# Performance work log

Hardware: AMD Instinct MI355X
Metric: run time of the kernel (lower is better)

## Reference

```python
import jax, jax.numpy as jnp
import numpy as np

EMBED_DIM = 1024
HEAD_DIM = 64
B, S = 4, 4096


def setup_inputs() -> dict:
    key = jax.random.key(0)
    ks = jax.random.split(key, 9)
    scale = 1.0 / np.sqrt(EMBED_DIM)
    return {
        "Q": jax.random.normal(ks[0], (B, S, EMBED_DIM), jnp.float32),
        "K": jax.random.normal(ks[1], (B, S, EMBED_DIM), jnp.float32),
        "V": jax.random.normal(ks[2], (B, S, EMBED_DIM), jnp.float32),
        "mask": jnp.ones((1, S, S), jnp.int32),
        "Wq": jax.random.normal(ks[3], (EMBED_DIM, HEAD_DIM), jnp.float32) * scale,
        "bq": jax.random.normal(ks[4], (HEAD_DIM,), jnp.float32) * scale,
        "Wk": jax.random.normal(ks[5], (EMBED_DIM, HEAD_DIM), jnp.float32) * scale,
        "bk": jax.random.normal(ks[6], (HEAD_DIM,), jnp.float32) * scale,
        "Wv": jax.random.normal(ks[7], (EMBED_DIM, HEAD_DIM), jnp.float32) * scale,
        "bv": jax.random.normal(ks[8], (HEAD_DIM,), jnp.float32) * scale,
    }


def reference(Q, K, V, mask, Wq, bq, Wk, bk, Wv, bv):
    # Per-head projections: [B,S,E] @ [E,D] -> [B,S,D]
    q = Q @ Wq + bq
    k = K @ Wk + bk
    v = V @ Wv + bv
    d_k = q.shape[-1]
    # scores: [B,Sq,Sk]
    scores = jnp.einsum("bqd,bkd->bqk", q, k) / jnp.sqrt(jnp.float32(d_k))
    scores = jnp.where(mask == 0, -jnp.inf, scores)
    p_attn = jax.nn.softmax(scores, axis=-1)
    return jnp.einsum("bqk,bkd->bqd", p_attn, v)
```

## Files before the change

### kernel.cpp

```cpp
#include <hip/hip_runtime.h>

#define B_ 4
#define S_ 4096
#define E_ 1024
#define D_ 64

typedef __attribute__((ext_vector_type(8))) short short8;
typedef __attribute__((ext_vector_type(4))) float floatx4;
typedef __attribute__((ext_vector_type(4))) unsigned int uint4v;

__device__ __forceinline__ floatx4 mfma_bf16(short8 a, short8 b, floatx4 c) {
    return __builtin_amdgcn_mfma_f32_16x16x32_bf16(a, b, c, 0, 0, 0);
}

__device__ __forceinline__ short f2bf(float f) {
    unsigned u = __builtin_bit_cast(unsigned, f);
    u = (u + 0x7FFFu + ((u >> 16) & 1u)) >> 16;
    return (short)u;
}

__device__ __forceinline__ unsigned pk2bf(float a, float b) {
    unsigned ua = __builtin_bit_cast(unsigned, a);
    unsigned ub = __builtin_bit_cast(unsigned, b);
    ua = (ua + 0x7FFFu + ((ua >> 16) & 1u)) >> 16;
    ub = (ub + 0x7FFFu + ((ub >> 16) & 1u)) & 0xFFFF0000u;
    return ua | ub;
}

__global__ __launch_bounds__(256) void prep_kernel(
    const float* __restrict__ Wq, const float* __restrict__ Wk, const float* __restrict__ Wv,
    short* __restrict__ WT, int* __restrict__ flag)
{
    int tid = blockIdx.x * 256 + threadIdx.x;
    if (tid == 0) *flag = 0;
    int mat = tid >> 16;
    int rem = tid & 65535;
    const float* W = (mat == 0) ? Wq : ((mat == 1) ? Wk : Wv);
    int n = rem >> 10, k = rem & 1023;
    WT[mat * 65536 + n * E_ + k] = f2bf(W[k * D_ + n]);
}

__global__ __launch_bounds__(256) void maskchk_kernel(
    const int4* __restrict__ mask4, int* __restrict__ flag)
{
    int tid = blockIdx.x * blockDim.x + threadIdx.x;
    int stride = gridDim.x * blockDim.x;
    int found = 0;
    for (int i = tid; i < (S_ * S_ / 4); i += stride) {
        int4 v = mask4[i];
        found |= (v.x == 0) | (v.y == 0) | (v.z == 0) | (v.w == 0);
    }
    if (found) atomicOr(flag, 1);
}

__global__ __launch_bounds__(256, 3) void proj_kernel(
    const float* __restrict__ Qm, const float* __restrict__ Km, const float* __restrict__ Vm,
    const short* __restrict__ WT,
    const float* __restrict__ bq, const float* __restrict__ bk, const float* __restrict__ bv,
    short* __restrict__ qs, short* __restrict__ ks, short* __restrict__ vT)
{
    const int mt = blockIdx.x;
    const int mat = blockIdx.y;
    const int wave = threadIdx.x >> 6;
    const int lane = threadIdx.x & 63;
    const int quad = lane >> 4, c16 = lane & 15;
    const int m0 = mt * 64 + wave * 16;

    const float* X    = (mat == 0) ? Qm : ((mat == 1) ? Km : Vm);
    const float* bias = (mat == 0) ? bq : ((mat == 1) ? bk : bv);
    const short* Wt   = WT + mat * (D_ * E_);

    const float* arow = X + (size_t)(m0 + c16) * E_ + quad * 8;

    floatx4 acc[4];
    #pragma unroll
    for (int f = 0; f < 4; ++f) acc[f] = (floatx4){0.f, 0.f, 0.f, 0.f};

    float4 pa[4], pb[4];
    #pragma unroll
    for (int j = 0; j < 4; ++j) {
        pa[j] = *(const float4*)(arow + j * 32);
        pb[j] = *(const float4*)(arow + j * 32 + 4);
    }

    #pragma unroll 4
    for (int it = 0; it < 32; ++it) {
        float4 ca = pa[it & 3], cb = pb[it & 3];
        if (it < 28) {
            pa[it & 3] = *(const float4*)(arow + (it + 4) * 32);
            pb[it & 3] = *(const float4*)(arow + (it + 4) * 32 + 4);
        }
        uint4v uv;
        uv[0] = pk2bf(ca.x, ca.y); uv[1] = pk2bf(ca.z, ca.w);
        uv[2] = pk2bf(cb.x, cb.y); uv[3] = pk2bf(cb.z, cb.w);
        short8 a = __builtin_bit_cast(short8, uv);
        #pragma unroll
        for (int f = 0; f < 4; ++f) {
            short8 bfr = *(const short8*)(Wt + (size_t)(f * 16 + c16) * E_ + it * 32 + quad * 8);
            acc[f] = mfma_bf16(a, bfr, acc[f]);
        }
    }

    const float scale = (mat == 0) ? (0.125f * 1.4426950408889634f) : 1.0f;
    #pragma unroll
    for (int f = 0; f < 4; ++f) {
        float bb = bias[f * 16 + c16];
        #pragma unroll
        for (int r = 0; r < 4; ++r) {
            int m = m0 + quad * 4 + r;
            float v = (acc[f][r] + bb) * scale;
            short h = f2bf(v);
            if (mat == 0)      qs[(size_t)m * D_ + f * 16 + c16] = h;
            else if (mat == 1) ks[(size_t)m * D_ + f * 16 + c16] = h;
            else vT[((size_t)((m >> 12) * D_ + f * 16 + c16)) * S_ + (m & (S_ - 1))] = h;
        }
    }
}

__global__ __launch_bounds__(512, 2) void flash_kernel(
    const short* __restrict__ qs, const short* __restrict__ ks,
    const short* __restrict__ vT, const int* __restrict__ mask,
    const int* __restrict__ flag, float* __restrict__ out)
{
    __shared__ __align__(16) char smem[35840];
    short* kst = (short*)smem;
    short* pst = kst + 9216;

    const int bid = blockIdx.x;
    const int b  = (bid & 7) >> 1;
    const int qt = ((bid >> 3) << 1) | (bid & 1);
    const int tid = threadIdx.x;
    const int w = tid >> 6;
    const int qw = w & 3, kw = w >> 2;
    const int lane = tid & 63;
    const int quad = lane >> 4, c16 = lane & 15;
    const int m0 = qt * 64 + qw * 16;

    const short* qrow = qs + (size_t)(b * S_ + m0 + c16) * D_ + quad * 8;
    short8 aq0 = *(const short8*)(qrow);
    short8 aq1 = *(const short8*)(qrow + 32);

    const short* kbase = ks + (size_t)b * S_ * D_ + (size_t)kw * 2048 * D_;
    const short* vbase = vT + (size_t)b * D_ * S_ + kw * 2048;

    const int srow = (w & 3) * 8 + (lane >> 3);
    const int schunk = lane & 7;
    const short* gstage = kbase + srow * D_ + schunk * 8;
    short* lstage = kst + kw * 2304 + srow * 72 + schunk * 8;

    floatx4 O[4];
    #pragma unroll
    for (int f = 0; f < 4; ++f) O[f] = (floatx4){0.f, 0.f, 0.f, 0.f};
    float lsum = 0.f;

    const int anyz = *flag;
    short* pw = pst + w * 640;
    short8 g = *(const short8*)(gstage);

    for (int kt = 0; kt < 64; ++kt) {
        const int buf = kt & 1;
        *(short8*)(lstage + buf * 4608) = g;
        short8 gn = g;
        if (kt < 63) gn = *(const short8*)(gstage + (size_t)(kt + 1) * 2048);
        __syncthreads();

        const int key0 = kt * 32;

        short8 vv[4];
        #pragma unroll
        for (int f = 0; f < 4; ++f)
            vv[f] = *(const short8*)(vbase + (size_t)(f * 16 + c16) * S_ + key0 + quad * 8);

        const short* kt_lds = kst + buf * 4608 + kw * 2304;

        floatx4 s[2];
        #pragma unroll
        for (int f = 0; f < 2; ++f) {
            const short* krow = kt_lds + (f * 16 + c16) * 72 + quad * 8;
            short8 ka0 = *(const short8*)(krow);
            short8 ka1 = *(const short8*)(krow + 32);
            floatx4 t = (floatx4){0.f, 0.f, 0.f, 0.f};
            t = mfma_bf16(ka0, aq0, t);
            t = mfma_bf16(ka1, aq1, t);
            s[f] = t;
        }

        if (anyz) {
            #pragma unroll
            for (int f = 0; f < 2; ++f)
                #pragma unroll
                for (int r = 0; r < 4; ++r)
                    if (mask[(size_t)(m0 + c16) * S_ +
                             kw * 2048 + key0 + f * 16 + quad * 4 + r] == 0)
                        s[f][r] = -__builtin_inff();
        }

        #pragma unroll
        for (int f = 0; f < 2; ++f) {
            float p0 = exp2f(s[f][0]), p1 = exp2f(s[f][1]);
            float p2 = exp2f(s[f][2]), p3 = exp2f(s[f][3]);
            lsum += (p0 + p1) + (p2 + p3);
            int2 pk = make_int2((int)pk2bf(p0, p1), (int)pk2bf(p2, p3));
            *(int2*)(pw + c16 * 40 + f * 16 + quad * 4) = pk;
        }

        short8 pa = *(const short8*)(pw + c16 * 40 + quad * 8);

        #pragma unroll
        for (int f = 0; f < 4; ++f) O[f] = mfma_bf16(pa, vv[f], O[f]);
        g = gn;
    }

    lsum += __shfl_xor(lsum, 16);
    lsum += __shfl_xor(lsum, 32);

    __syncthreads();
    float* of = (float*)smem;
    float* lw = (float*)(smem + 34816);
    #pragma unroll
    for (int f = 0; f < 4; ++f)
        #pragma unroll
        for (int r = 0; r < 4; ++r)
            of[(kw * 64 + qw * 16 + quad * 4 + r) * 68 + f * 16 + c16] = O[f][r];
    if (quad == 0) lw[kw * 64 + qw * 16 + c16] = lsum;
    __syncthreads();

    {
        const int q = tid >> 3;
        const int col0 = (tid & 7) * 8;
        const float inv = 1.0f / (lw[q] + lw[64 + q]);
        const float* r0 = &of[q * 68 + col0];
        const float* r1 = &of[(64 + q) * 68 + col0];
        float4 o0, o1;
        o0.x = (r0[0] + r1[0]) * inv; o0.y = (r0[1] + r1[1]) * inv;
        o0.z = (r0[2] + r1[2]) * inv; o0.w = (r0[3] + r1[3]) * inv;
        o1.x = (r0[4] + r1[4]) * inv; o1.y = (r0[5] + r1[5]) * inv;
        o1.z = (r0[6] + r1[6]) * inv; o1.w = (r0[7] + r1[7]) * inv;
        float* op = out + ((size_t)(b * S_ + qt * 64 + q)) * 64 + col0;
        *(float4*)(op) = o0;
        *(float4*)(op + 4) = o1;
    }
}

extern "C" void kernel_launch(void* const* d_in, const int* in_sizes, int n_in,
                              void* d_out, int out_size, void* d_ws, size_t ws_size,
                              hipStream_t stream)
{
    const float* Q   = (const float*)d_in[0];
    const float* K   = (const float*)d_in[1];
    const float* V   = (const float*)d_in[2];
    const int*  mask = (const int*) d_in[3];
    const float* Wq  = (const float*)d_in[4];
    const float* bq  = (const float*)d_in[5];
    const float* Wk  = (const float*)d_in[6];
    const float* bk  = (const float*)d_in[7];
    const float* Wv  = (const float*)d_in[8];
    const float* bv  = (const float*)d_in[9];
    float* out = (float*)d_out;

    short* qs = (short*)d_ws;
    short* ks = qs + (size_t)B_ * S_ * D_;
    short* vT = ks + (size_t)B_ * S_ * D_;
    short* WT = vT + (size_t)B_ * S_ * D_;
    int* flag = (int*)(WT + 3 * D_ * E_);

    prep_kernel<<<768, 256, 0, stream>>>(Wq, Wk, Wv, WT, flag);
    maskchk_kernel<<<2048, 256, 0, stream>>>((const int4*)mask, flag);
    proj_kernel<<<dim3(256, 3), 256, 0, stream>>>(Q, K, V, WT, bq, bk, bv, qs, ks, vT);
    flash_kernel<<<256, 512, 0, stream>>>(qs, ks, vT, mask, flag, out);
}
```

Before: 355.0 us.

## Stage projection tiles via global_load_lds double buffer and fold mask check into proj

Rewrites the projection kernel to stage A (fp32 activations) and W tiles into LDS with direct global-to-LDS loads, using double buffering with XOR-swizzled layouts. Each block now covers 32 rows, and the K dimension is split across wave pairs whose partial sums are reduced through LDS. The separate mask-check kernel is merged in as an extra grid row, which removes one launch and lets the check overlap with projection work. In exchange the kernel now uses more shared memory, needs a barrier every stage and an extra reduction step, and the swizzle indexing is a correctness risk.

```diff
diff --git a/kernel.cpp b/kernel.cpp
--- a/kernel.cpp
+++ b/kernel.cpp
@@ -25,6 +25,12 @@
     ua = (ua + 0x7FFFu + ((ua >> 16) & 1u)) >> 16;
     ub = (ub + 0x7FFFu + ((ub >> 16) & 1u)) & 0xFFFF0000u;
     return ua | ub;
+}
+
+__device__ __forceinline__ void gload_lds16(const void* g, void* l) {
+    __builtin_amdgcn_global_load_lds(
+        (const __attribute__((address_space(1))) void*)g,
+        (__attribute__((address_space(3))) void*)l, 16, 0, 0);
 }
 
 __global__ __launch_bounds__(256) void prep_kernel(
@@ -40,79 +46,116 @@
     WT[mat * 65536 + n * E_ + k] = f2bf(W[k * D_ + n]);
 }
 
-__global__ __launch_bounds__(256) void maskchk_kernel(
-    const int4* __restrict__ mask4, int* __restrict__ flag)
-{
-    int tid = blockIdx.x * blockDim.x + threadIdx.x;
-    int stride = gridDim.x * blockDim.x;
-    int found = 0;
-    for (int i = tid; i < (S_ * S_ / 4); i += stride) {
-        int4 v = mask4[i];
-        found |= (v.x == 0) | (v.y == 0) | (v.z == 0) | (v.w == 0);
-    }
-    if (found) atomicOr(flag, 1);
-}
-
-__global__ __launch_bounds__(256, 3) void proj_kernel(
+__global__ __launch_bounds__(256, 4) void proj_kernel(
     const float* __restrict__ Qm, const float* __restrict__ Km, const float* __restrict__ Vm,
     const short* __restrict__ WT,
     const float* __restrict__ bq, const float* __restrict__ bk, const float* __restrict__ bv,
-    short* __restrict__ qs, short* __restrict__ ks, short* __restrict__ vT)
+    short* __restrict__ qs, short* __restrict__ ks, short* __restrict__ vT,
+    const int4* __restrict__ mask4, int* __restrict__ flag)
 {
-    const int mt = blockIdx.x;
+    if (blockIdx.y == 3) {
+        int tid = blockIdx.x * 256 + threadIdx.x;
+        const int stride = 512 * 256;
+        int found = 0;
+        for (int i = tid; i < (S_ * S_ / 4); i += stride) {
+            int4 v = mask4[i];
+            found |= (v.x == 0) | (v.y == 0) | (v.z == 0) | (v.w == 0);
+        }
+        if (found) atomicOr(flag, 1);
+        return;
+    }
+
+    __shared__ __align__(16) char smem[32768];
+
     const int mat = blockIdx.y;
-    const int wave = threadIdx.x >> 6;
-    const int lane = threadIdx.x & 63;
+    const int bx  = blockIdx.x;
+    const int tid = threadIdx.x;
+    const int w = tid >> 6, lane = tid & 63;
+    const int rt = w & 1, kh = w >> 1;
     const int quad = lane >> 4, c16 = lane & 15;
-    const int m0 = mt * 64 + wave * 16;
+    const int row0 = bx * 32;
 
     const float* X    = (mat == 0) ? Qm : ((mat == 1) ? Km : Vm);
     const float* bias = (mat == 0) ? bq : ((mat == 1) ? bk : bv);
-    const short* Wt   = WT + mat * (D_ * E_);
-
-    const float* arow = X + (size_t)(m0 + c16) * E_ + quad * 8;
+
+    const int slot = w * 64 + lane;
+    const int arow = slot >> 3, ac = slot & 7;
+    const int acs  = ac ^ (arow & 7);
+    const char* gA = (const char*)X + (size_t)(row0 + arow) * 4096 + (size_t)acs * 16;
+    const int wn = slot >> 2, wc = slot & 3;
+    const int wcs = wc ^ ((wn >> 1) & 3);
+    const char* gW = (const char*)(WT + (size_t)mat * 65536) + (size_t)wn * 2048 + (size_t)wcs * 16;
+
+    char* lw = smem + w * 1024;
+
+    #define PSTAGE(buf, s) do {                                   \
+        const char* a0 = gA + (s) * 128;                          \
+        const char* w0 = gW + (s) * 64;                           \
+        char* lb = lw + (buf) * 16384;                            \
+        gload_lds16(a0,        lb);                               \
+        gload_lds16(a0 + 2048, lb + 4096);                        \
+        gload_lds16(w0,        lb + 8192);                        \
+        gload_lds16(w0 + 1024, lb + 12288);                       \
+    } while (0)
 
     floatx4 acc[4];
     #pragma unroll
     for (int f = 0; f < 4; ++f) acc[f] = (floatx4){0.f, 0.f, 0.f, 0.f};
 
-    float4 pa[4], pb[4];
-    #pragma unroll
-    for (int j = 0; j < 4; ++j) {
-        pa[j] = *(const float4*)(arow + j * 32);
-        pb[j] = *(const float4*)(arow + j * 32 + 4);
-    }
-
-    #pragma unroll 4
-    for (int it = 0; it < 32; ++it) {
-        float4 ca = pa[it & 3], cb = pb[it & 3];
-        if (it < 28) {
-            pa[it & 3] = *(const float4*)(arow + (it + 4) * 32);
-            pb[it & 3] = *(const float4*)(arow + (it + 4) * 32 + 4);
-        }
+    const int am = c16 & 7;
+    const int wm = (c16 >> 1) & 3;
+    const char* aAbase = smem + kh * 4096 + (rt * 16 + c16) * 128;
+    const char* aWbase = smem + 8192 + kh * 4096 + c16 * 64 + ((quad ^ wm)) * 16;
+
+    PSTAGE(0, 0);
+    __syncthreads();
+
+    #pragma unroll 2
+    for (int s = 0; s < 16; ++s) {
+        const int buf = s & 1;
+        if (s < 15) PSTAGE(buf ^ 1, s + 1);
+
+        const char* aA = aAbase + buf * 16384;
+        float4 fa = *(const float4*)(aA + (size_t)(((2 * quad)     ^ am) * 16));
+        float4 fb = *(const float4*)(aA + (size_t)(((2 * quad + 1) ^ am) * 16));
         uint4v uv;
-        uv[0] = pk2bf(ca.x, ca.y); uv[1] = pk2bf(ca.z, ca.w);
-        uv[2] = pk2bf(cb.x, cb.y); uv[3] = pk2bf(cb.z, cb.w);
+        uv[0] = pk2bf(fa.x, fa.y); uv[1] = pk2bf(fa.z, fa.w);
+        uv[2] = pk2bf(fb.x, fb.y); uv[3] = pk2bf(fb.z, fb.w);
         short8 a = __builtin_bit_cast(short8, uv);
+
+        const char* aW = aWbase + buf * 16384;
         #pragma unroll
         for (int f = 0; f < 4; ++f) {
-            short8 bfr = *(const short8*)(Wt + (size_t)(f * 16 + c16) * E_ + it * 32 + quad * 8);
-            acc[f] = mfma_bf16(a, bfr, acc[f]);
-        }
-    }
-
-    const float scale = (mat == 0) ? (0.125f * 1.4426950408889634f) : 1.0f;
-    #pragma unroll
-    for (int f = 0; f < 4; ++f) {
-        float bb = bias[f * 16 + c16];
-        #pragma unroll
-        for (int r = 0; r < 4; ++r) {
-            int m = m0 + quad * 4 + r;
-            float v = (acc[f][r] + bb) * scale;
-            short h = f2bf(v);
-            if (mat == 0)      qs[(size_t)m * D_ + f * 16 + c16] = h;
-            else if (mat == 1) ks[(size_t)m * D_ + f * 16 + c16] = h;
-            else vT[((size_t)((m >> 12) * D_ + f * 16 + c16)) * S_ + (m & (S_ - 1))] = h;
+            short8 b = *(const short8*)(aW + (size_t)(f * 16) * 64);
+            acc[f] = mfma_bf16(a, b, acc[f]);
+        }
+        __syncthreads();
+    }
+    #undef PSTAGE
+
+    float* of = (float*)smem;
+    if (kh == 1) {
+        #pragma unroll
+        for (int f = 0; f < 4; ++f)
+            #pragma unroll
+            for (int r = 0; r < 4; ++r)
+                of[(rt * 16 + quad * 4 + r) * 68 + f * 16 + c16] = acc[f][r];
+    }
+    __syncthreads();
+    if (kh == 0) {
+        const float scale = (mat == 0) ? (0.125f * 1.4426950408889634f) : 1.0f;
+        #pragma unroll
+        for (int f = 0; f < 4; ++f) {
+            float bb = bias[f * 16 + c16];
+            #pragma unroll
+            for (int r = 0; r < 4; ++r) {
+                int m = row0 + rt * 16 + quad * 4 + r;
+                float v = (acc[f][r] + of[(rt * 16 + quad * 4 + r) * 68 + f * 16 + c16] + bb) * scale;
+                short h = f2bf(v);
+                if (mat == 0)      qs[(size_t)m * D_ + f * 16 + c16] = h;
+                else if (mat == 1) ks[(size_t)m * D_ + f * 16 + c16] = h;
+                else vT[((size_t)((m >> 12) * D_ + f * 16 + c16)) * S_ + (m & (S_ - 1))] = h;
+            }
         }
     }
 }
@@ -265,7 +308,7 @@
     int* flag = (int*)(WT + 3 * D_ * E_);
 
     prep_kernel<<<768, 256, 0, stream>>>(Wq, Wk, Wv, WT, flag);
-    maskchk_kernel<<<2048, 256, 0, stream>>>((const int4*)mask, flag);
-    proj_kernel<<<dim3(256, 3), 256, 0, stream>>>(Q, K, V, WT, bq, bk, bv, qs, ks, vT);
+    proj_kernel<<<dim3(512, 4), 256, 0, stream>>>(Q, K, V, WT, bq, bk, bv,
+                                                  qs, ks, vT, (const int4*)mask, flag);
     flash_kernel<<<256, 512, 0, stream>>>(qs, ks, vT, mask, flag, out);
 }
```

Measured after the change: 334.5 us. -5.8%, faster.

## Stage projection inputs through LDS with async loads and fuse mask check

Applied to the files above, without the earlier changes.

The projection kernel now streams the fp32 activation rows into a swizzled LDS ring buffer using global_load_lds with a three-stage prefetch and explicit vmcnt waits. Weight fragments are double-buffered in registers. The separate mask-check kernel is folded into the tail of the projection kernel, which removes one launch. Occupancy is raised to 4 blocks per SM. The trade-off is added LDS use and a hand-tuned waitcnt that depends on the exact number of loads in flight.

```diff
diff --git a/kernel.cpp b/kernel.cpp
--- a/kernel.cpp
+++ b/kernel.cpp
@@ -25,6 +25,12 @@
     ua = (ua + 0x7FFFu + ((ua >> 16) & 1u)) >> 16;
     ub = (ub + 0x7FFFu + ((ub >> 16) & 1u)) & 0xFFFF0000u;
     return ua | ub;
+}
+
+__device__ __forceinline__ void gload_lds16(const void* g, void* l) {
+    __builtin_amdgcn_global_load_lds(
+        (const __attribute__((address_space(1))) void*)g,
+        (__attribute__((address_space(3))) void*)l, 16, 0, 0);
 }
 
 __global__ __launch_bounds__(256) void prep_kernel(
@@ -40,66 +46,85 @@
     WT[mat * 65536 + n * E_ + k] = f2bf(W[k * D_ + n]);
 }
 
-__global__ __launch_bounds__(256) void maskchk_kernel(
-    const int4* __restrict__ mask4, int* __restrict__ flag)
-{
-    int tid = blockIdx.x * blockDim.x + threadIdx.x;
-    int stride = gridDim.x * blockDim.x;
-    int found = 0;
-    for (int i = tid; i < (S_ * S_ / 4); i += stride) {
-        int4 v = mask4[i];
-        found |= (v.x == 0) | (v.y == 0) | (v.z == 0) | (v.w == 0);
-    }
-    if (found) atomicOr(flag, 1);
-}
-
-__global__ __launch_bounds__(256, 3) void proj_kernel(
+__global__ __launch_bounds__(256, 4) void proj_kernel(
     const float* __restrict__ Qm, const float* __restrict__ Km, const float* __restrict__ Vm,
     const short* __restrict__ WT,
     const float* __restrict__ bq, const float* __restrict__ bk, const float* __restrict__ bv,
-    short* __restrict__ qs, short* __restrict__ ks, short* __restrict__ vT)
+    short* __restrict__ qs, short* __restrict__ ks, short* __restrict__ vT,
+    const int4* __restrict__ mask4, int* __restrict__ flag)
 {
-    const int mt = blockIdx.x;
+    __shared__ __align__(16) char smem[32768];
+
     const int mat = blockIdx.y;
-    const int wave = threadIdx.x >> 6;
-    const int lane = threadIdx.x & 63;
+    const int bx  = blockIdx.x;
+    const int tid = threadIdx.x;
+    const int wv = tid >> 6, lane = tid & 63;
     const int quad = lane >> 4, c16 = lane & 15;
-    const int m0 = mt * 64 + wave * 16;
+    const int m0 = bx * 64 + wv * 16;
 
     const float* X    = (mat == 0) ? Qm : ((mat == 1) ? Km : Vm);
     const float* bias = (mat == 0) ? bq : ((mat == 1) ? bk : bv);
-    const short* Wt   = WT + mat * (D_ * E_);
-
-    const float* arow = X + (size_t)(m0 + c16) * E_ + quad * 8;
+    const short* Wt   = WT + mat * 65536;
+
+    const int srow = lane >> 3;
+    const int cs   = (lane & 7) ^ srow;
+    const char* gA = (const char*)X + (size_t)(m0 + srow) * 4096 + (size_t)cs * 16;
+    char* lds_w = smem + wv * 8192;
+
+    #define PSTAGE(s) do {                               \
+        const char* a0_ = gA + (size_t)(s) * 128;        \
+        char* lb_ = lds_w + ((s) & 3) * 2048;            \
+        gload_lds16(a0_,         lb_);                   \
+        gload_lds16(a0_ + 32768, lb_ + 1024);            \
+    } while (0)
+
+    const short* wbase = Wt + (size_t)c16 * 1024 + quad * 8;
+    #define WLOAD(s, dst) do {                           \
+        const short* wp_ = wbase + (s) * 32;             \
+        dst[0] = *(const short8*)(wp_);                  \
+        dst[1] = *(const short8*)(wp_ + 16384);          \
+        dst[2] = *(const short8*)(wp_ + 32768);          \
+        dst[3] = *(const short8*)(wp_ + 49152);          \
+    } while (0)
 
     floatx4 acc[4];
     #pragma unroll
     for (int f = 0; f < 4; ++f) acc[f] = (floatx4){0.f, 0.f, 0.f, 0.f};
-
-    float4 pa[4], pb[4];
-    #pragma unroll
-    for (int j = 0; j < 4; ++j) {
-        pa[j] = *(const float4*)(arow + j * 32);
-        pb[j] = *(const float4*)(arow + j * 32 + 4);
-    }
-
-    #pragma unroll 4
-    for (int it = 0; it < 32; ++it) {
-        float4 ca = pa[it & 3], cb = pb[it & 3];
-        if (it < 28) {
-            pa[it & 3] = *(const float4*)(arow + (it + 4) * 32);
-            pb[it & 3] = *(const float4*)(arow + (it + 4) * 32 + 4);
-        }
+    short8 wA[4], wB[4];
+
+    PSTAGE(0); PSTAGE(1); PSTAGE(2);
+    WLOAD(0, wA); WLOAD(1, wB);
+
+    const int am = c16 & 7;
+    const char* ra = smem + wv * 8192 + c16 * 128;
+    const int off0 = ((2 * quad)     ^ am) * 16;
+    const int off1 = ((2 * quad + 1) ^ am) * 16;
+
+    #pragma unroll 2
+    for (int s = 0; s < 32; ++s) {
+        asm volatile("s_waitcnt vmcnt(12)" ::: "memory");
+        if (s + 3 < 32) PSTAGE(s + 3);
+
+        const char* rb = ra + (s & 3) * 2048;
+        float4 fa = *(const float4*)(rb + off0);
+        float4 fb = *(const float4*)(rb + off1);
         uint4v uv;
-        uv[0] = pk2bf(ca.x, ca.y); uv[1] = pk2bf(ca.z, ca.w);
-        uv[2] = pk2bf(cb.x, cb.y); uv[3] = pk2bf(cb.z, cb.w);
+        uv[0] = pk2bf(fa.x, fa.y); uv[1] = pk2bf(fa.z, fa.w);
+        uv[2] = pk2bf(fb.x, fb.y); uv[3] = pk2bf(fb.z, fb.w);
         short8 a = __builtin_bit_cast(short8, uv);
-        #pragma unroll
-        for (int f = 0; f < 4; ++f) {
-            short8 bfr = *(const short8*)(Wt + (size_t)(f * 16 + c16) * E_ + it * 32 + quad * 8);
-            acc[f] = mfma_bf16(a, bfr, acc[f]);
-        }
-    }
+
+        if (s & 1) {
+            #pragma unroll
+            for (int f = 0; f < 4; ++f) acc[f] = mfma_bf16(a, wB[f], acc[f]);
+            if (s + 2 < 32) WLOAD(s + 2, wB);
+        } else {
+            #pragma unroll
+            for (int f = 0; f < 4; ++f) acc[f] = mfma_bf16(a, wA[f], acc[f]);
+            if (s + 2 < 32) WLOAD(s + 2, wA);
+        }
+    }
+    #undef PSTAGE
+    #undef WLOAD
 
     const float scale = (mat == 0) ? (0.125f * 1.4426950408889634f) : 1.0f;
     #pragma unroll
@@ -114,6 +139,17 @@
             else if (mat == 1) ks[(size_t)m * D_ + f * 16 + c16] = h;
             else vT[((size_t)((m >> 12) * D_ + f * 16 + c16)) * S_ + (m & (S_ - 1))] = h;
         }
+    }
+
+    {
+        int btid = (mat * 256 + bx) * 256 + tid;
+        const int stride = 768 * 256;
+        int found = 0;
+        for (int i = btid; i < (S_ * S_ / 4); i += stride) {
+            int4 v = mask4[i];
+            found |= (v.x == 0) | (v.y == 0) | (v.z == 0) | (v.w == 0);
+        }
+        if (found) atomicOr(flag, 1);
     }
 }
 
@@ -265,7 +301,7 @@
     int* flag = (int*)(WT + 3 * D_ * E_);
 
     prep_kernel<<<768, 256, 0, stream>>>(Wq, Wk, Wv, WT, flag);
-    maskchk_kernel<<<2048, 256, 0, stream>>>((const int4*)mask, flag);
-    proj_kernel<<<dim3(256, 3), 256, 0, stream>>>(Q, K, V, WT, bq, bk, bv, qs, ks, vT);
+    proj_kernel<<<dim3(256, 3), 256, 0, stream>>>(Q, K, V, WT, bq, bk, bv,
+                                                  qs, ks, vT, (const int4*)mask, flag);
     flash_kernel<<<256, 512, 0, stream>>>(qs, ks, vT, mask, flag, out);
 }
```

Measured after the change: 348.3 us. Within noise of the previous version (-1.9%).

## Fuse mask check into projection, split-K projection and 4-way key split in flash

Applied to the files above, without the earlier changes.

Removes the separate mask-scan kernel and folds the scan into the tail of the projection kernel. The projection now uses 32-row tiles with a two-way split of the reduction dimension across waves, combined through shared memory, which doubles the block count. The attention kernel now uses 32-query tiles with keys split four ways per block, 512 blocks in total, and a four-way final reduction. The goal is more parallelism and one fewer launch, at the cost of extra LDS traffic and a larger shared-memory footprint.

```diff
diff --git a/kernel.cpp b/kernel.cpp
--- a/kernel.cpp
+++ b/kernel.cpp
@@ -40,80 +40,83 @@
     WT[mat * 65536 + n * E_ + k] = f2bf(W[k * D_ + n]);
 }
 
-__global__ __launch_bounds__(256) void maskchk_kernel(
-    const int4* __restrict__ mask4, int* __restrict__ flag)
-{
-    int tid = blockIdx.x * blockDim.x + threadIdx.x;
-    int stride = gridDim.x * blockDim.x;
-    int found = 0;
-    for (int i = tid; i < (S_ * S_ / 4); i += stride) {
-        int4 v = mask4[i];
-        found |= (v.x == 0) | (v.y == 0) | (v.z == 0) | (v.w == 0);
-    }
-    if (found) atomicOr(flag, 1);
-}
-
-__global__ __launch_bounds__(256, 3) void proj_kernel(
+__global__ __launch_bounds__(256, 4) void proj_kernel(
     const float* __restrict__ Qm, const float* __restrict__ Km, const float* __restrict__ Vm,
     const short* __restrict__ WT,
     const float* __restrict__ bq, const float* __restrict__ bk, const float* __restrict__ bv,
-    short* __restrict__ qs, short* __restrict__ ks, short* __restrict__ vT)
-{
-    const int mt = blockIdx.x;
+    short* __restrict__ qs, short* __restrict__ ks, short* __restrict__ vT,
+    const int4* __restrict__ mask4, int* __restrict__ flag)
+{
+    __shared__ __align__(16) float of[32 * 68];
+
     const int mat = blockIdx.y;
-    const int wave = threadIdx.x >> 6;
-    const int lane = threadIdx.x & 63;
+    const int bx  = blockIdx.x;
+    const int tid = threadIdx.x;
+    const int wv = tid >> 6, lane = tid & 63;
     const int quad = lane >> 4, c16 = lane & 15;
-    const int m0 = mt * 64 + wave * 16;
+    const int rt = wv & 1, kh = wv >> 1;
+    const int m0 = bx * 32 + rt * 16;
 
     const float* X    = (mat == 0) ? Qm : ((mat == 1) ? Km : Vm);
     const float* bias = (mat == 0) ? bq : ((mat == 1) ? bk : bv);
-    const short* Wt   = WT + mat * (D_ * E_);
-
-    const float* arow = X + (size_t)(m0 + c16) * E_ + quad * 8;
+    const short* Wt   = WT + mat * 65536;
+
+    const float* arow = X + (size_t)(m0 + c16) * E_ + kh * 512 + quad * 8;
+    const short* wbase = Wt + (size_t)c16 * E_ + kh * 512 + quad * 8;
 
     floatx4 acc[4];
     #pragma unroll
     for (int f = 0; f < 4; ++f) acc[f] = (floatx4){0.f, 0.f, 0.f, 0.f};
 
-    float4 pa[4], pb[4];
-    #pragma unroll
-    for (int j = 0; j < 4; ++j) {
-        pa[j] = *(const float4*)(arow + j * 32);
-        pb[j] = *(const float4*)(arow + j * 32 + 4);
-    }
-
     #pragma unroll 4
-    for (int it = 0; it < 32; ++it) {
-        float4 ca = pa[it & 3], cb = pb[it & 3];
-        if (it < 28) {
-            pa[it & 3] = *(const float4*)(arow + (it + 4) * 32);
-            pb[it & 3] = *(const float4*)(arow + (it + 4) * 32 + 4);
-        }
+    for (int it = 0; it < 16; ++it) {
+        float4 fa = *(const float4*)(arow + it * 32);
+        float4 fb = *(const float4*)(arow + it * 32 + 4);
         uint4v uv;
-        uv[0] = pk2bf(ca.x, ca.y); uv[1] = pk2bf(ca.z, ca.w);
-        uv[2] = pk2bf(cb.x, cb.y); uv[3] = pk2bf(cb.z, cb.w);
+        uv[0] = pk2bf(fa.x, fa.y); uv[1] = pk2bf(fa.z, fa.w);
+        uv[2] = pk2bf(fb.x, fb.y); uv[3] = pk2bf(fb.z, fb.w);
         short8 a = __builtin_bit_cast(short8, uv);
         #pragma unroll
         for (int f = 0; f < 4; ++f) {
-            short8 bfr = *(const short8*)(Wt + (size_t)(f * 16 + c16) * E_ + it * 32 + quad * 8);
-            acc[f] = mfma_bf16(a, bfr, acc[f]);
-        }
-    }
-
-    const float scale = (mat == 0) ? (0.125f * 1.4426950408889634f) : 1.0f;
-    #pragma unroll
-    for (int f = 0; f < 4; ++f) {
-        float bb = bias[f * 16 + c16];
-        #pragma unroll
-        for (int r = 0; r < 4; ++r) {
-            int m = m0 + quad * 4 + r;
-            float v = (acc[f][r] + bb) * scale;
-            short h = f2bf(v);
-            if (mat == 0)      qs[(size_t)m * D_ + f * 16 + c16] = h;
-            else if (mat == 1) ks[(size_t)m * D_ + f * 16 + c16] = h;
-            else vT[((size_t)((m >> 12) * D_ + f * 16 + c16)) * S_ + (m & (S_ - 1))] = h;
-        }
+            short8 b = *(const short8*)(wbase + (size_t)f * 16384 + it * 32);
+            acc[f] = mfma_bf16(a, b, acc[f]);
+        }
+    }
+
+    if (kh == 1) {
+        #pragma unroll
+        for (int f = 0; f < 4; ++f)
+            #pragma unroll
+            for (int r = 0; r < 4; ++r)
+                of[(rt * 16 + quad * 4 + r) * 68 + f * 16 + c16] = acc[f][r];
+    }
+    __syncthreads();
+    if (kh == 0) {
+        const float scale = (mat == 0) ? (0.125f * 1.4426950408889634f) : 1.0f;
+        #pragma unroll
+        for (int f = 0; f < 4; ++f) {
+            float bb = bias[f * 16 + c16];
+            #pragma unroll
+            for (int r = 0; r < 4; ++r) {
+                int m = m0 + quad * 4 + r;
+                float v = (acc[f][r] + of[(rt * 16 + quad * 4 + r) * 68 + f * 16 + c16] + bb) * scale;
+                short h = f2bf(v);
+                if (mat == 0)      qs[(size_t)m * D_ + f * 16 + c16] = h;
+                else if (mat == 1) ks[(size_t)m * D_ + f * 16 + c16] = h;
+                else vT[((size_t)((m >> 12) * D_ + f * 16 + c16)) * S_ + (m & (S_ - 1))] = h;
+            }
+        }
+    }
+
+    {
+        int btid = (mat * 512 + bx) * 256 + tid;
+        const int stride = 1536 * 256;
+        int found = 0;
+        for (int i = btid; i < (S_ * S_ / 4); i += stride) {
+            int4 v = mask4[i];
+            found |= (v.x == 0) | (v.y == 0) | (v.z == 0) | (v.w == 0);
+        }
+        if (found) atomicOr(flag, 1);
     }
 }
 
@@ -122,31 +125,32 @@
     const short* __restrict__ vT, const int* __restrict__ mask,
     const int* __restrict__ flag, float* __restrict__ out)
 {
-    __shared__ __align__(16) char smem[35840];
+    __shared__ __align__(16) char smem[47104];
     short* kst = (short*)smem;
-    short* pst = kst + 9216;
+    short* pst = kst + 18432;
 
     const int bid = blockIdx.x;
     const int b  = (bid & 7) >> 1;
     const int qt = ((bid >> 3) << 1) | (bid & 1);
     const int tid = threadIdx.x;
     const int w = tid >> 6;
-    const int qw = w & 3, kw = w >> 2;
+    const int qw = w & 1, kwq = w >> 1;
     const int lane = tid & 63;
     const int quad = lane >> 4, c16 = lane & 15;
-    const int m0 = qt * 64 + qw * 16;
+    const int m0 = qt * 32 + qw * 16;
 
     const short* qrow = qs + (size_t)(b * S_ + m0 + c16) * D_ + quad * 8;
     short8 aq0 = *(const short8*)(qrow);
     short8 aq1 = *(const short8*)(qrow + 32);
 
-    const short* kbase = ks + (size_t)b * S_ * D_ + (size_t)kw * 2048 * D_;
-    const short* vbase = vT + (size_t)b * D_ * S_ + kw * 2048;
-
-    const int srow = (w & 3) * 8 + (lane >> 3);
+    const short* kbase = ks + (size_t)b * S_ * D_;
+    const short* vbase = vT + (size_t)b * D_ * S_ + kwq * 1024;
+
+    const int sq   = w >> 1;
+    const int srow = (w & 1) * 16 + (lane >> 3);
     const int schunk = lane & 7;
-    const short* gstage = kbase + srow * D_ + schunk * 8;
-    short* lstage = kst + kw * 2304 + srow * 72 + schunk * 8;
+    const short* gstage = kbase + ((size_t)sq * 1024 + srow) * D_ + schunk * 8;
+    short* lstage = kst + sq * 2304 + srow * 72 + schunk * 8;
 
     floatx4 O[4];
     #pragma unroll
@@ -155,13 +159,18 @@
 
     const int anyz = *flag;
     short* pw = pst + w * 640;
-    short8 g = *(const short8*)(gstage);
-
-    for (int kt = 0; kt < 64; ++kt) {
+    short8 g0 = *(const short8*)(gstage);
+    short8 g1 = *(const short8*)(gstage + 8 * D_);
+
+    for (int kt = 0; kt < 32; ++kt) {
         const int buf = kt & 1;
-        *(short8*)(lstage + buf * 4608) = g;
-        short8 gn = g;
-        if (kt < 63) gn = *(const short8*)(gstage + (size_t)(kt + 1) * 2048);
+        *(short8*)(lstage + buf * 9216)           = g0;
+        *(short8*)(lstage + buf * 9216 + 8 * 72)  = g1;
+        short8 gn0 = g0, gn1 = g1;
+        if (kt < 31) {
+            gn0 = *(const short8*)(gstage + (size_t)(kt + 1) * 2048);
+            gn1 = *(const short8*)(gstage + (size_t)(kt + 1) * 2048 + 8 * D_);
+        }
         __syncthreads();
 
         const int key0 = kt * 32;
@@ -171,7 +180,7 @@
         for (int f = 0; f < 4; ++f)
             vv[f] = *(const short8*)(vbase + (size_t)(f * 16 + c16) * S_ + key0 + quad * 8);
 
-        const short* kt_lds = kst + buf * 4608 + kw * 2304;
+        const short* kt_lds = kst + buf * 9216 + kwq * 2304;
 
         floatx4 s[2];
         #pragma unroll
@@ -191,7 +200,7 @@
                 #pragma unroll
                 for (int r = 0; r < 4; ++r)
                     if (mask[(size_t)(m0 + c16) * S_ +
-                             kw * 2048 + key0 + f * 16 + quad * 4 + r] == 0)
+                             kwq * 1024 + key0 + f * 16 + quad * 4 + r] == 0)
                         s[f][r] = -__builtin_inff();
         }
 
@@ -208,7 +217,7 @@
 
         #pragma unroll
         for (int f = 0; f < 4; ++f) O[f] = mfma_bf16(pa, vv[f], O[f]);
-        g = gn;
+        g0 = gn0; g1 = gn1;
     }
 
     lsum += __shfl_xor(lsum, 16);
@@ -221,24 +230,22 @@
     for (int f = 0; f < 4; ++f)
         #pragma unroll
         for (int r = 0; r < 4; ++r)
-            of[(kw * 64 + qw * 16 + quad * 4 + r) * 68 + f * 16 + c16] = O[f][r];
-    if (quad == 0) lw[kw * 64 + qw * 16 + c16] = lsum;
+            of[(kwq * 32 + qw * 16 + quad * 4 + r) * 68 + f * 16 + c16] = O[f][r];
+    if (quad == 0) lw[kwq * 32 + qw * 16 + c16] = lsum;
     __syncthreads();
 
     {
-        const int q = tid >> 3;
-        const int col0 = (tid & 7) * 8;
-        const float inv = 1.0f / (lw[q] + lw[64 + q]);
-        const float* r0 = &of[q * 68 + col0];
-        const float* r1 = &of[(64 + q) * 68 + col0];
-        float4 o0, o1;
-        o0.x = (r0[0] + r1[0]) * inv; o0.y = (r0[1] + r1[1]) * inv;
-        o0.z = (r0[2] + r1[2]) * inv; o0.w = (r0[3] + r1[3]) * inv;
-        o1.x = (r0[4] + r1[4]) * inv; o1.y = (r0[5] + r1[5]) * inv;
-        o1.z = (r0[6] + r1[6]) * inv; o1.w = (r0[7] + r1[7]) * inv;
-        float* op = out + ((size_t)(b * S_ + qt * 64 + q)) * 64 + col0;
-        *(float4*)(op) = o0;
-        *(float4*)(op + 4) = o1;
+        const int q = tid >> 4;
+        const int col0 = (tid & 15) * 4;
+        const float inv = 1.0f / (lw[q] + lw[32 + q] + lw[64 + q] + lw[96 + q]);
+        float4 o = *(const float4*)&of[q * 68 + col0];
+        #pragma unroll
+        for (int k = 1; k < 4; ++k) {
+            float4 t = *(const float4*)&of[(k * 32 + q) * 68 + col0];
+            o.x += t.x; o.y += t.y; o.z += t.z; o.w += t.w;
+        }
+        o.x *= inv; o.y *= inv; o.z *= inv; o.w *= inv;
+        *(float4*)(out + ((size_t)(b * S_ + qt * 32 + q)) * 64 + col0) = o;
     }
 }
 
@@ -265,7 +272,7 @@
     int* flag = (int*)(WT + 3 * D_ * E_);
 
     prep_kernel<<<768, 256, 0, stream>>>(Wq, Wk, Wv, WT, flag);
-    maskchk_kernel<<<2048, 256, 0, stream>>>((const int4*)mask, flag);
-    proj_kernel<<<dim3(256, 3), 256, 0, stream>>>(Q, K, V, WT, bq, bk, bv, qs, ks, vT);
-    flash_kernel<<<256, 512, 0, stream>>>(qs, ks, vT, mask, flag, out);
-}
+    proj_kernel<<<dim3(512, 3), 256, 0, stream>>>(Q, K, V, WT, bq, bk, bv,
+                                                  qs, ks, vT, (const int4*)mask, flag);
+    flash_kernel<<<512, 512, 0, stream>>>(qs, ks, vT, mask, flag, out);
+}
```

After: 345.3 us. -2.8%, faster.
